# Kernel optimization log

Hardware: AMD Instinct MI355X
Metric: run time of the kernel (lower is better)

The kernel has to match this reference:

```python
import jax, jax.numpy as jnp
import numpy as np

D_EMB = 1024
D_ATTN = 1024
NUM_HEADS = 16
HEAD_DIM = D_ATTN // NUM_HEADS
SEQ = 2048
BS = 2


def setup_inputs() -> dict:
    key = jax.random.key(0)
    ks = jax.random.split(key, 6)
    s = 1.0 / np.sqrt(D_EMB)
    return {
        "x": jax.random.normal(ks[0], (BS, SEQ, D_EMB), dtype=jnp.float32),
        "W_q": jax.random.uniform(ks[1], (D_ATTN, D_EMB), jnp.float32, -s, s),
        "W_k": jax.random.uniform(ks[2], (D_ATTN, D_EMB), jnp.float32, -s, s),
        "W_v": jax.random.uniform(ks[3], (D_ATTN, D_EMB), jnp.float32, -s, s),
        "W_o": jax.random.uniform(ks[4], (D_ATTN, D_ATTN), jnp.float32, -s, s),
        "b_o": jax.random.uniform(ks[5], (D_ATTN,), jnp.float32, -s, s),
    }


def reference(x, W_q, W_k, W_v, W_o, b_o):
    bs, seq_len, _ = x.shape
    # QKV projections (torch Linear: x @ W.T)
    q = jnp.einsum('bse,ae->bsa', x, W_q).reshape(bs, seq_len, NUM_HEADS, HEAD_DIM)
    k = jnp.einsum('bse,ae->bsa', x, W_k).reshape(bs, seq_len, NUM_HEADS, HEAD_DIM)
    v = jnp.einsum('bse,ae->bsa', x, W_v).reshape(bs, seq_len, NUM_HEADS, HEAD_DIM)
    # [b, h, s, d]
    q = q.transpose(0, 2, 1, 3)
    k = k.transpose(0, 2, 1, 3)
    v = v.transpose(0, 2, 1, 3)
    # scores [b, h, s, s] with causal mask
    scores = jnp.einsum('bhqd,bhkd->bhqk', q, k)
    causal = jnp.tril(jnp.ones((seq_len, seq_len), dtype=bool))
    scores = jnp.where(causal, scores, -jnp.inf)
    attn = jax.nn.softmax(scores / np.sqrt(HEAD_DIM), axis=-1)
    # dropout p=0.0 -> identity
    ctx = jnp.einsum('bhqk,bhkd->bhqd', attn, v)
    ctx = ctx.transpose(0, 2, 1, 3).reshape(bs, seq_len, D_ATTN)
    return jnp.einsum('bsa,oa->bso', ctx, W_o) + b_o
```

## Files before the change

### kernel.cpp

```cpp
#include <hip/hip_runtime.h>
#include <stdint.h>

#define SEQ   2048
#define DEMB  1024
#define NH    16
#define HD    64
#define MROWS 4096

typedef __bf16 bf16x8 __attribute__((ext_vector_type(8)));
typedef __bf16 bf16x4 __attribute__((ext_vector_type(4)));
typedef float  f32x4  __attribute__((ext_vector_type(4)));

#define MFMA(a, b, c) __builtin_amdgcn_mfma_f32_16x16x32_bf16((a), (b), (c), 0, 0, 0)

static __device__ __forceinline__ uint16_t f2bf(float f) {
  union { __bf16 b; uint16_t u; } c;
  c.b = (__bf16)f;
  return c.u;
}

static __device__ __forceinline__ ushort4 pack4(f32x4 f) {
  union { bf16x4 b; ushort4 u; } c;
  c.b[0] = (__bf16)f[0]; c.b[1] = (__bf16)f[1];
  c.b[2] = (__bf16)f[2]; c.b[3] = (__bf16)f[3];
  return c.u;
}

static __device__ __forceinline__ bf16x8 ldb8(const uint16_t* p) {
  union { uint4 i; bf16x8 b; } u;
  u.i = *(const uint4*)p;
  return u.b;
}

static __device__ __forceinline__ void gld_lds16(const uint16_t* g, uint16_t* l) {
  __builtin_amdgcn_global_load_lds(
      (const __attribute__((address_space(1))) uint32_t*)(g),
      (__attribute__((address_space(3))) uint32_t*)(l),
      16, 0, 0);
}

__global__ __launch_bounds__(256) void cvt_all(const float* __restrict__ x,
                                               const float* __restrict__ wq,
                                               const float* __restrict__ wk,
                                               const float* __restrict__ wv,
                                               const float* __restrict__ wo,
                                               uint16_t* __restrict__ xb,
                                               uint16_t* __restrict__ wqkv,
                                               uint16_t* __restrict__ wob) {
  const int bid = blockIdx.x;
  const float* src; uint16_t* dst; int off;
  if (bid < 4096)      { src = x;  dst = xb;                 off = bid; }
  else if (bid < 5120) { src = wq; dst = wqkv;               off = bid - 4096; }
  else if (bid < 6144) { src = wk; dst = wqkv + (1u << 20);  off = bid - 5120; }
  else if (bid < 7168) { src = wv; dst = wqkv + (2u << 20);  off = bid - 6144; }
  else                 { src = wo; dst = wob;                off = bid - 7168; }
  const int i = (off * 256 + threadIdx.x) * 4;
  float4 v = *(const float4*)(src + i);
  f32x4 f; f[0] = v.x; f[1] = v.y; f[2] = v.z; f[3] = v.w;
  *(ushort4*)(dst + i) = pack4(f);
}

template <int MODE>
__global__ __launch_bounds__(512, 4) void gemm_bt(const uint16_t* __restrict__ A,
                                                  const uint16_t* __restrict__ B,
                                                  uint16_t* __restrict__ Cq,
                                                  uint16_t* __restrict__ Ck,
                                                  uint16_t* __restrict__ Cvt,
                                                  float* __restrict__ Cf,
                                                  const float* __restrict__ bias) {
  constexpr int K  = 1024;
  constexpr int BN = (MODE == 0) ? 192 : 64;
  constexpr int NI = (MODE == 0) ? 3 : 1;

  __shared__ uint16_t As[2][128 * 64];
  __shared__ uint16_t Bs[2][BN * 64];

  const int brow = blockIdx.y << 7;
  const int bcol = blockIdx.x * BN;

  const int t  = threadIdx.x;
  const int l  = t & 63;
  const int li = l & 15, lg = l >> 4;
  const int w  = t >> 6;
  const int wm = w >> 2;
  const int wn = w & 3;

  const int srow = t >> 3;
  const int scol = ((t & 7) ^ (srow & 7)) << 3;
  const uint16_t* gA = A + (size_t)(brow + srow) * K + scol;
  const uint16_t* gB = B + (size_t)(bcol + srow) * K + scol;

  auto stage = [&](int buf, int k0) {
    gld_lds16(gA + k0, &As[buf][t * 8]);
    gld_lds16(gA + (size_t)64 * K + k0, &As[buf][4096 + t * 8]);
    gld_lds16(gB + k0, &Bs[buf][t * 8]);
    if (MODE == 0) {
      gld_lds16(gB + (size_t)64 * K + k0,  &Bs[buf][4096 + t * 8]);
      gld_lds16(gB + (size_t)128 * K + k0, &Bs[buf][8192 + t * 8]);
    }
  };

  const int sw = li & 7;
  auto ldA = [&](int buf, int kh, int fi) {
    const int row = wm * 64 + fi * 16 + li;
    return ldb8(&As[buf][(row << 6) + ((((kh << 2) + lg) ^ sw) << 3)]);
  };
  auto ldB = [&](int buf, int kh, int ni) {
    const int row = wn * (BN / 4) + ni * 16 + li;
    return ldb8(&Bs[buf][(row << 6) + ((((kh << 2) + lg) ^ sw) << 3)]);
  };

  f32x4 acc[4][NI] = {};

  stage(0, 0);
  __syncthreads();
  int cur = 0;

  for (int k0 = 0; k0 < K; k0 += 64) {
    if (k0 + 64 < K) stage(cur ^ 1, k0 + 64);

#pragma unroll
    for (int kh = 0; kh < 2; ++kh) {
      bf16x8 af[4], bfr[NI];
#pragma unroll
      for (int fi = 0; fi < 4; ++fi) af[fi] = ldA(cur, kh, fi);
#pragma unroll
      for (int ni = 0; ni < NI; ++ni) bfr[ni] = ldB(cur, kh, ni);
      __builtin_amdgcn_s_setprio(1);
#pragma unroll
      for (int fi = 0; fi < 4; ++fi)
#pragma unroll
        for (int ni = 0; ni < NI; ++ni)
          acc[fi][ni] = MFMA(af[fi], bfr[ni], acc[fi][ni]);
      __builtin_amdgcn_s_setprio(0);
    }

    __syncthreads();
    cur ^= 1;
  }

#pragma unroll
  for (int mi = 0; mi < 4; ++mi) {
#pragma unroll
    for (int ni = 0; ni < NI; ++ni) {
      const int row = brow + wm * 64 + mi * 16 + lg * 4;
      const int col = bcol + wn * (BN / 4) + ni * 16 + li;
#pragma unroll
      for (int r = 0; r < 4; ++r) {
        const float v = acc[mi][ni][r];
        if (MODE == 0) {
          if (col < 1024) {
            Cq[(size_t)(row + r) * 1024 + col] = f2bf(v * 0.18033688f);
          } else if (col < 2048) {
            Ck[(size_t)(row + r) * 1024 + (col - 1024)] = f2bf(v);
          } else {
            const int c = col - 2048;
            const int m = row + r;
            Cvt[((size_t)c + (size_t)((m >> 11) << 10)) * 2048 + (m & 2047)] = f2bf(v);
          }
        } else {
          Cf[(size_t)(row + r) * 1024 + col] = v + bias[col];
        }
      }
    }
  }
}

__global__ __launch_bounds__(256, 3) void attn_fwd(const uint16_t* __restrict__ Q,
                                                   const uint16_t* __restrict__ K,
                                                   const uint16_t* __restrict__ Vt,
                                                   uint16_t* __restrict__ ctx) {
  const int id   = blockIdx.x;
  const int rank = id >> 3;
  const int bh   = (id & 7) * 4 + (rank >> 4);
  const int pr   = rank & 15;
  const int b = bh >> 4, h = bh & 15;

  const int t  = threadIdx.x;
  const int w  = t >> 6, l = t & 63;
  const int li = l & 15, lg = l >> 4;

  __shared__ uint16_t Kl[2][64 * 64];
  __shared__ uint16_t Vl[2][64 * 64];
  __shared__ uint16_t P[4][16][72];

  const uint16_t* Kg = K + (size_t)(b * 2048) * 1024 + h * 64;
  const uint16_t* Vg = Vt + (size_t)(b * 1024 + h * 64) * 2048;

  const int srow = t >> 3;
  const int scol = ((t & 7) * 8) ^ ((srow & 7) * 8);

  auto stage = [&](int buf, int kt2) {
    const int kb2 = kt2 << 6;
    gld_lds16(Kg + (size_t)(kb2 + srow) * 1024 + scol,      &Kl[buf][t * 8]);
    gld_lds16(Kg + (size_t)(kb2 + 32 + srow) * 1024 + scol, &Kl[buf][2048 + t * 8]);
    gld_lds16(Vg + (size_t)srow * 2048 + kb2 + scol,        &Vl[buf][t * 8]);
    gld_lds16(Vg + (size_t)(32 + srow) * 2048 + kb2 + scol, &Vl[buf][2048 + t * 8]);
  };

  const int fsw = (li & 7) * 8;
  int cur = 0;

#pragma unroll 1
  for (int ph = 0; ph < 2; ++ph) {
    const int qbl  = ph ? (31 - pr) : pr;
    const int qrow = (qbl << 6) + (w << 4);
    const uint16_t* qp = Q + (size_t)(b * 2048 + qrow + li) * 1024 + h * 64 + lg * 8;
    const bf16x8 q0 = ldb8(qp);
    const bf16x8 q1 = ldb8(qp + 32);

    f32x4 o[4] = {};
    float l_r = 0.f;

    stage(cur, 0);
    __syncthreads();

    for (int kt = 0; kt <= qbl; ++kt) {
      if (kt < qbl) stage(cur ^ 1, kt + 1);

      const uint16_t* Kc = &Kl[cur][0];
      const uint16_t* Vc = &Vl[cur][0];

      f32x4 s[4];
      __builtin_amdgcn_s_setprio(1);
#pragma unroll
      for (int tt = 0; tt < 4; ++tt) {
        const uint16_t* kr = Kc + (tt * 16 + li) * 64;
        f32x4 z = {};
        z = MFMA(ldb8(kr + ((lg * 8) ^ fsw)), q0, z);
        z = MFMA(ldb8(kr + ((32 + lg * 8) ^ fsw)), q1, z);
        s[tt] = z;
      }
      __builtin_amdgcn_s_setprio(0);

      bf16x8 vf[4][2];
#pragma unroll
      for (int dt = 0; dt < 4; ++dt) {
        const uint16_t* vr = Vc + (dt * 16 + li) * 64;
        vf[dt][0] = ldb8(vr + ((lg * 8) ^ fsw));
        vf[dt][1] = ldb8(vr + ((32 + lg * 8) ^ fsw));
      }

      if (kt == qbl) {
        const int qloc = (w << 4) + li;
#pragma unroll
        for (int tt = 0; tt < 4; ++tt) {
          const int key = (tt << 4) + (lg << 2);
#pragma unroll
          for (int r = 0; r < 4; ++r)
            if (key + r > qloc) s[tt][r] = -1e30f;
        }
      }

      float lsum = 0.f;
      ushort4 pk[4];
#pragma unroll
      for (int tt = 0; tt < 4; ++tt) {
        f32x4 p;
        p[0] = __builtin_amdgcn_exp2f(s[tt][0]);
        p[1] = __builtin_amdgcn_exp2f(s[tt][1]);
        p[2] = __builtin_amdgcn_exp2f(s[tt][2]);
        p[3] = __builtin_amdgcn_exp2f(s[tt][3]);
        lsum += (p[0] + p[1]) + (p[2] + p[3]);
        pk[tt] = pack4(p);
      }
      l_r += lsum;

#pragma unroll
      for (int tt = 0; tt < 4; ++tt)
        *(ushort4*)&P[w][li][(tt << 4) + (lg << 2)] = pk[tt];
      asm volatile("s_waitcnt lgkmcnt(0)" ::: "memory");

      const bf16x8 pb0 = ldb8(&P[w][li][lg * 8]);
      const bf16x8 pb1 = ldb8(&P[w][li][32 + lg * 8]);
      __builtin_amdgcn_s_setprio(1);
#pragma unroll
      for (int dt = 0; dt < 4; ++dt) {
        o[dt] = MFMA(vf[dt][0], pb0, o[dt]);
        o[dt] = MFMA(vf[dt][1], pb1, o[dt]);
      }
      __builtin_amdgcn_s_setprio(0);

      __syncthreads();
      cur ^= 1;
    }

    l_r += __shfl_xor(l_r, 16);
    l_r += __shfl_xor(l_r, 32);
    const float inv = 1.0f / l_r;
    const int qg = b * 2048 + qrow + li;
#pragma unroll
    for (int dt = 0; dt < 4; ++dt) {
      f32x4 ov = o[dt];
      ov[0] *= inv; ov[1] *= inv; ov[2] *= inv; ov[3] *= inv;
      *(ushort4*)(ctx + (size_t)qg * 1024 + h * 64 + (dt << 4) + (lg << 2)) = pack4(ov);
    }
  }
}

extern "C" void kernel_launch(void* const* d_in, const int* in_sizes, int n_in,
                              void* d_out, int out_size, void* d_ws, size_t ws_size,
                              hipStream_t stream) {
  const float* x  = (const float*)d_in[0];
  const float* Wq = (const float*)d_in[1];
  const float* Wk = (const float*)d_in[2];
  const float* Wv = (const float*)d_in[3];
  const float* Wo = (const float*)d_in[4];
  const float* bo = (const float*)d_in[5];
  float* out = (float*)d_out;

  char* ws = (char*)d_ws;
  uint16_t* xb   = (uint16_t*)(ws);
  uint16_t* Wqkv = (uint16_t*)(ws + ( 8u << 20));
  uint16_t* Wob  = (uint16_t*)(ws + (14u << 20));
  uint16_t* Qb   = (uint16_t*)(ws + (16u << 20));
  uint16_t* Kb   = (uint16_t*)(ws + (24u << 20));
  uint16_t* Vt   = (uint16_t*)(ws + (32u << 20));
  uint16_t* Ctx  = (uint16_t*)(ws);

  cvt_all<<<8192, 256, 0, stream>>>(x, Wq, Wk, Wv, Wo, xb, Wqkv, Wob);

  gemm_bt<0><<<dim3(16, 32), 512, 0, stream>>>(xb, Wqkv, Qb, Kb, Vt,
                                               nullptr, nullptr);

  attn_fwd<<<512, 256, 0, stream>>>(Qb, Kb, Vt, Ctx);

  gemm_bt<2><<<dim3(16, 32), 512, 0, stream>>>(Ctx, Wob, nullptr, nullptr, nullptr,
                                               out, bo);
}
```

Before: 109.0 us.

## Enlarge GEMM tiles and stage V-transpose stores through LDS

The QKV GEMM moves to 256x192 tiles with 8x3 MFMA fragments per wave, which halves the grid and raises operand reuse. The transposed V output is first written into a per-wave LDS slab and then stored to global memory as 16-byte vectors instead of scattered 2-byte writes. The output projection GEMM moves from 128x64 to 128x128 tiles and loads each bias value once. The cost is more LDS and registers per block, lower occupancy (launch bounds of 2) and fewer blocks, which may underfill the CUs (256 and 256 blocks).

```diff
diff --git a/kernel.cpp b/kernel.cpp
--- a/kernel.cpp
+++ b/kernel.cpp
@@ -60,23 +60,16 @@
   *(ushort4*)(dst + i) = pack4(f);
 }
 
-template <int MODE>
-__global__ __launch_bounds__(512, 4) void gemm_bt(const uint16_t* __restrict__ A,
-                                                  const uint16_t* __restrict__ B,
-                                                  uint16_t* __restrict__ Cq,
-                                                  uint16_t* __restrict__ Ck,
-                                                  uint16_t* __restrict__ Cvt,
-                                                  float* __restrict__ Cf,
-                                                  const float* __restrict__ bias) {
-  constexpr int K  = 1024;
-  constexpr int BN = (MODE == 0) ? 192 : 64;
-  constexpr int NI = (MODE == 0) ? 3 : 1;
-
-  __shared__ uint16_t As[2][128 * 64];
-  __shared__ uint16_t Bs[2][BN * 64];
-
-  const int brow = blockIdx.y << 7;
-  const int bcol = blockIdx.x * BN;
+__global__ __launch_bounds__(512, 2) void gemm_qkv(const uint16_t* __restrict__ A,
+                                                   const uint16_t* __restrict__ B,
+                                                   uint16_t* __restrict__ Cq,
+                                                   uint16_t* __restrict__ Ck,
+                                                   uint16_t* __restrict__ Cvt) {
+  constexpr int K = 1024;
+  __shared__ uint16_t lds[57344];
+
+  const int bcol = blockIdx.x * 192;
+  const int brow = blockIdx.y << 8;
 
   const int t  = threadIdx.x;
   const int l  = t & 63;
@@ -91,13 +84,125 @@
   const uint16_t* gB = B + (size_t)(bcol + srow) * K + scol;
 
   auto stage = [&](int buf, int k0) {
-    gld_lds16(gA + k0, &As[buf][t * 8]);
+    uint16_t* as = lds + buf * 16384;
+    uint16_t* bs = lds + 32768 + buf * 12288;
+    gld_lds16(gA + k0,                    as + t * 8);
+    gld_lds16(gA + (size_t)64 * K + k0,   as + 4096 + t * 8);
+    gld_lds16(gA + (size_t)128 * K + k0,  as + 8192 + t * 8);
+    gld_lds16(gA + (size_t)192 * K + k0,  as + 12288 + t * 8);
+    gld_lds16(gB + k0,                    bs + t * 8);
+    gld_lds16(gB + (size_t)64 * K + k0,   bs + 4096 + t * 8);
+    gld_lds16(gB + (size_t)128 * K + k0,  bs + 8192 + t * 8);
+  };
+
+  const int sw = li & 7;
+  auto ldA = [&](int buf, int kh, int fi) {
+    const int row = wm * 128 + fi * 16 + li;
+    return ldb8(&lds[buf * 16384 + (row << 6) + ((((kh << 2) + lg) ^ sw) << 3)]);
+  };
+  auto ldB = [&](int buf, int kh, int ni) {
+    const int row = wn * 48 + ni * 16 + li;
+    return ldb8(&lds[32768 + buf * 12288 + (row << 6) + ((((kh << 2) + lg) ^ sw) << 3)]);
+  };
+
+  f32x4 acc[8][3] = {};
+
+  stage(0, 0);
+  __syncthreads();
+  int cur = 0;
+
+  for (int k0 = 0; k0 < K; k0 += 64) {
+    if (k0 + 64 < K) stage(cur ^ 1, k0 + 64);
+
+#pragma unroll
+    for (int kh = 0; kh < 2; ++kh) {
+      bf16x8 af[8], bfr[3];
+#pragma unroll
+      for (int ni = 0; ni < 3; ++ni) bfr[ni] = ldB(cur, kh, ni);
+#pragma unroll
+      for (int fi = 0; fi < 8; ++fi) af[fi] = ldA(cur, kh, fi);
+      __builtin_amdgcn_s_setprio(1);
+#pragma unroll
+      for (int fi = 0; fi < 8; ++fi)
+#pragma unroll
+        for (int ni = 0; ni < 3; ++ni)
+          acc[fi][ni] = MFMA(af[fi], bfr[ni], acc[fi][ni]);
+      __builtin_amdgcn_s_setprio(0);
+    }
+
+    __syncthreads();
+    cur ^= 1;
+  }
+
+  uint16_t* slab = lds + w * 6800;
+  bool anyV = false;
+
+#pragma unroll
+  for (int mi = 0; mi < 8; ++mi) {
+#pragma unroll
+    for (int ni = 0; ni < 3; ++ni) {
+      const int col = bcol + wn * 48 + ni * 16 + li;
+      const int row = brow + wm * 128 + mi * 16 + lg * 4;
+      if (col < 1024) {
+#pragma unroll
+        for (int r = 0; r < 4; ++r)
+          Cq[(size_t)(row + r) * 1024 + col] = f2bf(acc[mi][ni][r] * 0.18033688f);
+      } else if (col < 2048) {
+#pragma unroll
+        for (int r = 0; r < 4; ++r)
+          Ck[(size_t)(row + r) * 1024 + (col - 1024)] = f2bf(acc[mi][ni][r]);
+      } else {
+        anyV = true;
+        *(ushort4*)&slab[(ni * 16 + li) * 136 + mi * 16 + lg * 4] = pack4(acc[mi][ni]);
+      }
+    }
+  }
+
+  if (anyV) {
+    asm volatile("s_waitcnt lgkmcnt(0)" ::: "memory");
+    const int m0 = brow + wm * 128;
+    const size_t mbase = (size_t)((m0 >> 11) << 10) * 2048 + (m0 & 2047);
+#pragma unroll
+    for (int cc = 0; cc < 12; ++cc) {
+      const int c_loc = cc * 4 + lg;
+      const int cglob = bcol + wn * 48 + c_loc;
+      if (cglob >= 2048) {
+        const int c = cglob - 2048;
+        uint4 v = *(const uint4*)&slab[c_loc * 136 + li * 8];
+        *(uint4*)(Cvt + (size_t)c * 2048 + mbase + li * 8) = v;
+      }
+    }
+  }
+}
+
+__global__ __launch_bounds__(512, 2) void gemm_out(const uint16_t* __restrict__ A,
+                                                   const uint16_t* __restrict__ B,
+                                                   float* __restrict__ Cf,
+                                                   const float* __restrict__ bias) {
+  constexpr int K = 1024;
+  __shared__ uint16_t As[2][128 * 64];
+  __shared__ uint16_t Bs[2][128 * 64];
+
+  const int bcol = blockIdx.x << 7;
+  const int brow = blockIdx.y << 7;
+
+  const int t  = threadIdx.x;
+  const int l  = t & 63;
+  const int li = l & 15, lg = l >> 4;
+  const int w  = t >> 6;
+  const int wm = w >> 2;
+  const int wn = w & 3;
+
+  const int srow = t >> 3;
+  const int scol = ((t & 7) ^ (srow & 7)) << 3;
+  const uint16_t* gA = A + (size_t)(brow + srow) * K + scol;
+  const uint16_t* gB = B + (size_t)(bcol + srow) * K + scol;
+
+  auto stage = [&](int buf, int k0) {
+    gld_lds16(gA + k0,                  &As[buf][t * 8]);
     gld_lds16(gA + (size_t)64 * K + k0, &As[buf][4096 + t * 8]);
-    gld_lds16(gB + k0, &Bs[buf][t * 8]);
-    if (MODE == 0) {
-      gld_lds16(gB + (size_t)64 * K + k0,  &Bs[buf][4096 + t * 8]);
-      gld_lds16(gB + (size_t)128 * K + k0, &Bs[buf][8192 + t * 8]);
-    }
+    gld_lds16(gB + k0,                  &Bs[buf][t * 8]);
+    gld_lds16(gB + (size_t)64 * K + k0, &Bs[buf][4096 + t * 8]);
   };
 
   const int sw = li & 7;
@@ -106,11 +211,11 @@
     return ldb8(&As[buf][(row << 6) + ((((kh << 2) + lg) ^ sw) << 3)]);
   };
   auto ldB = [&](int buf, int kh, int ni) {
-    const int row = wn * (BN / 4) + ni * 16 + li;
+    const int row = wn * 32 + ni * 16 + li;
     return ldb8(&Bs[buf][(row << 6) + ((((kh << 2) + lg) ^ sw) << 3)]);
   };
 
-  f32x4 acc[4][NI] = {};
+  f32x4 acc[4][2] = {};
 
   stage(0, 0);
   __syncthreads();
@@ -121,16 +226,16 @@
 
 #pragma unroll
     for (int kh = 0; kh < 2; ++kh) {
-      bf16x8 af[4], bfr[NI];
+      bf16x8 af[4], bfr[2];
+#pragma unroll
+      for (int ni = 0; ni < 2; ++ni) bfr[ni] = ldB(cur, kh, ni);
 #pragma unroll
       for (int fi = 0; fi < 4; ++fi) af[fi] = ldA(cur, kh, fi);
-#pragma unroll
-      for (int ni = 0; ni < NI; ++ni) bfr[ni] = ldB(cur, kh, ni);
       __builtin_amdgcn_s_setprio(1);
 #pragma unroll
       for (int fi = 0; fi < 4; ++fi)
 #pragma unroll
-        for (int ni = 0; ni < NI; ++ni)
+        for (int ni = 0; ni < 2; ++ni)
           acc[fi][ni] = MFMA(af[fi], bfr[ni], acc[fi][ni]);
       __builtin_amdgcn_s_setprio(0);
     }
@@ -142,26 +247,13 @@
 #pragma unroll
   for (int mi = 0; mi < 4; ++mi) {
 #pragma unroll
-    for (int ni = 0; ni < NI; ++ni) {
+    for (int ni = 0; ni < 2; ++ni) {
       const int row = brow + wm * 64 + mi * 16 + lg * 4;
-      const int col = bcol + wn * (BN / 4) + ni * 16 + li;
-#pragma unroll
-      for (int r = 0; r < 4; ++r) {
-        const float v = acc[mi][ni][r];
-        if (MODE == 0) {
-          if (col < 1024) {
-            Cq[(size_t)(row + r) * 1024 + col] = f2bf(v * 0.18033688f);
-          } else if (col < 2048) {
-            Ck[(size_t)(row + r) * 1024 + (col - 1024)] = f2bf(v);
-          } else {
-            const int c = col - 2048;
-            const int m = row + r;
-            Cvt[((size_t)c + (size_t)((m >> 11) << 10)) * 2048 + (m & 2047)] = f2bf(v);
-          }
-        } else {
-          Cf[(size_t)(row + r) * 1024 + col] = v + bias[col];
-        }
-      }
+      const int col = bcol + wn * 32 + ni * 16 + li;
+      const float bv = bias[col];
+#pragma unroll
+      for (int r = 0; r < 4; ++r)
+        Cf[(size_t)(row + r) * 1024 + col] = acc[mi][ni][r] + bv;
     }
   }
 }
@@ -320,11 +412,9 @@
 
   cvt_all<<<8192, 256, 0, stream>>>(x, Wq, Wk, Wv, Wo, xb, Wqkv, Wob);
 
-  gemm_bt<0><<<dim3(16, 32), 512, 0, stream>>>(xb, Wqkv, Qb, Kb, Vt,
-                                               nullptr, nullptr);
+  gemm_qkv<<<dim3(16, 16), 512, 0, stream>>>(xb, Wqkv, Qb, Kb, Vt);
 
   attn_fwd<<<512, 256, 0, stream>>>(Qb, Kb, Vt, Ctx);
 
-  gemm_bt<2><<<dim3(16, 32), 512, 0, stream>>>(Ctx, Wob, nullptr, nullptr, nullptr,
-                                               out, bo);
-}
+  gemm_out<<<dim3(8, 32), 512, 0, stream>>>(Ctx, Wob, out, bo);
+}
```

New measurement: 99.12 us. 9.0% less time.
